# Kernel optimization log

Hardware: AMD Instinct MI355X
Metric: run time of the kernel (lower is better)

The kernel has to match this reference:

```python
import jax, jax.numpy as jnp
import numpy as np

NUM_HEADS = 16

def setup_inputs() -> dict:
    key = jax.random.key(0)
    ks = jax.random.split(key, 5)
    b, c, w, h = 2, 1024, 48, 48
    sc = 0.02
    return {
        "x": jax.random.normal(ks[0], (b, c, w, h), jnp.float32),
        "Wqkv": jax.random.normal(ks[1], (3 * c, c), jnp.float32) * sc,
        "bqkv": jax.random.normal(ks[2], (3 * c,), jnp.float32) * sc,
        "Wo": jax.random.normal(ks[3], (c, c), jnp.float32) * sc,
        "bo": jax.random.normal(ks[4], (c,), jnp.float32) * sc,
    }

def reference(x, Wqkv, bqkv, Wo, bo):
    b, c, w, h = x.shape
    n = NUM_HEADS
    hd = c // n
    s = w * h
    # [b,c,w,h] -> tokens [b, s, c]
    xs = x.transpose(0, 2, 3, 1).reshape(b, s, c)
    qkv = xs @ Wqkv.T + bqkv                       # [b, s, 3c]
    # rearrange 'b s (three n hd) -> three b n s hd'
    qkv = qkv.reshape(b, s, 3, n, hd).transpose(2, 0, 3, 1, 4)
    q, k, v = qkv[0], qkv[1], qkv[2]               # [b, n, s, hd]
    score = jnp.einsum('bnqh,bnkh->bnqk', q, k) / jnp.sqrt(jnp.float32(hd))
    # module uses a soft causal mask: subtract 10000 above the diagonal
    mask = 10000.0 * jnp.triu(jnp.ones((s, s), dtype=score.dtype), k=1)
    attn = jax.nn.softmax(score - mask, axis=-1)   # [b, n, s, s]
    z = jnp.einsum('bnqk,bnkh->bqnh', attn, v).reshape(b, s, c)
    out = z @ Wo.T + bo                            # [b, s, c]
    return out.reshape(b, w, h, c).transpose(0, 3, 1, 2)
```

## Files before the change

kernel.cpp:

```cpp
#include <hip/hip_runtime.h>

typedef __bf16 bf16;
typedef __bf16 bf16x8 __attribute__((ext_vector_type(8)));
typedef float floatx4 __attribute__((ext_vector_type(4)));
typedef float floatx16 __attribute__((ext_vector_type(16)));

static constexpr int S = 2304;
static constexpr int C = 1024;
static constexpr int NHEAD = 16;
static constexpr int HDIM = 64;
static constexpr int BATCH = 2;
static constexpr float QSCALE = 0.18033688011112042f;
static constexpr int QSPLIT = 18;
static constexpr int NACC = S - QSPLIT * 64;

__global__ __launch_bounds__(256) void k_zero(float4* __restrict__ p, int n4) {
  int i = blockIdx.x * 256 + threadIdx.x;
  if (i < n4) p[i] = float4{0.f, 0.f, 0.f, 0.f};
}

__global__ __launch_bounds__(256) void k_convert(const float* __restrict__ src,
                                                 bf16* __restrict__ dst, int n8) {
  int i = blockIdx.x * 256 + threadIdx.x;
  if (i >= n8) return;
  float4 a = *(const float4*)(src + (size_t)i * 8);
  float4 b = *(const float4*)(src + (size_t)i * 8 + 4);
  bf16x8 o;
  o[0] = (bf16)a.x; o[1] = (bf16)a.y; o[2] = (bf16)a.z; o[3] = (bf16)a.w;
  o[4] = (bf16)b.x; o[5] = (bf16)b.y; o[6] = (bf16)b.z; o[7] = (bf16)b.w;
  *(bf16x8*)(dst + (size_t)i * 8) = o;
}

__global__ __launch_bounds__(256) void k_transpose(const float* __restrict__ x,
                                                   bf16* __restrict__ xs) {
  __shared__ bf16 T[64 * 72];
  int c0 = blockIdx.x * 64, t0 = blockIdx.y * 64, b = blockIdx.z;
  int tid = threadIdx.x;
  const float* xb = x + (size_t)b * C * S;
#pragma unroll
  for (int it = 0; it < 4; ++it) {
    int idx = it * 256 + tid;
    int rc = idx >> 4, t4 = idx & 15;
    float4 v = *(const float4*)(xb + (size_t)(c0 + rc) * S + t0 + t4 * 4);
    T[(t4 * 4 + 0) * 72 + rc] = (bf16)v.x;
    T[(t4 * 4 + 1) * 72 + rc] = (bf16)v.y;
    T[(t4 * 4 + 2) * 72 + rc] = (bf16)v.z;
    T[(t4 * 4 + 3) * 72 + rc] = (bf16)v.w;
  }
  __syncthreads();
  bf16* xsb = xs + (size_t)b * S * C;
#pragma unroll
  for (int it = 0; it < 2; ++it) {
    int idx = it * 256 + tid;
    int rt = idx >> 3, c8 = idx & 7;
    bf16x8 v;
#pragma unroll
    for (int i = 0; i < 8; ++i) v[i] = T[rt * 72 + c8 * 8 + i];
    *(bf16x8*)(xsb + (size_t)(t0 + rt) * C + c0 + c8 * 8) = v;
  }
}

__device__ __forceinline__ void g2l16(const bf16* g, bf16* l) {
  __builtin_amdgcn_global_load_lds(
      (const __attribute__((address_space(1))) void*)g,
      (__attribute__((address_space(3))) void*)l, 16, 0, 0);
}

__device__ __forceinline__ unsigned cvtpk(float a, float b) {
  unsigned r;
  asm("v_cvt_pk_bf16_f32 %0, %1, %2" : "=v"(r) : "v"(a), "v"(b));
  return r;
}

__device__ __forceinline__ void pl32(unsigned& a, unsigned& b) {
  asm("v_permlane32_swap_b32 %0, %1" : "+v"(a), "+v"(b));
}

template <int EPI>
__global__ __launch_bounds__(256) void k_gemm_bt(const bf16* __restrict__ A,
                                                 const bf16* __restrict__ Bt,
                                                 const float* __restrict__ bias,
                                                 bf16* __restrict__ q,
                                                 bf16* __restrict__ k,
                                                 bf16* __restrict__ v,
                                                 float* __restrict__ outf) {
  constexpr int K = C;
  __shared__ bf16 As[128 * 64];
  __shared__ bf16 Bs[128 * 64];
  int tid = threadIdx.x;
  int w = tid >> 6, lane = tid & 63, ln = lane & 15, quad = lane >> 4;
  int m0 = blockIdx.y * 128, n0 = blockIdx.x * 128;
  int moff = (w >> 1) * 64, noff = (w & 1) * 64;
  floatx4 acc[4][4] = {};

  int sr[4], sc[4];
#pragma unroll
  for (int it = 0; it < 4; ++it) {
    int L = (it * 4 + w) * 64 + lane;
    sr[it] = L >> 3;
    sc[it] = (L & 7) ^ (sr[it] & 7);
  }

  for (int k0 = 0; k0 < K; k0 += 64) {
    __syncthreads();
#pragma unroll
    for (int it = 0; it < 4; ++it) {
      int cb = (it * 4 + w) * 64;
      g2l16(A + (size_t)(m0 + sr[it]) * K + k0 + sc[it] * 8, As + cb * 8);
      g2l16(Bt + (size_t)(n0 + sr[it]) * K + k0 + sc[it] * 8, Bs + cb * 8);
    }
    __syncthreads();
#pragma unroll
    for (int t = 0; t < 2; ++t) {
      bf16x8 af[4], bfr[4];
#pragma unroll
      for (int i = 0; i < 4; ++i) {
        int ra = moff + i * 16 + ln;
        af[i]  = *(const bf16x8*)(As + ra * 64 + (((t * 4 + quad) ^ (ra & 7))) * 8);
        int rb = noff + i * 16 + ln;
        bfr[i] = *(const bf16x8*)(Bs + rb * 64 + (((t * 4 + quad) ^ (rb & 7))) * 8);
      }
#pragma unroll
      for (int im = 0; im < 4; ++im)
#pragma unroll
        for (int in = 0; in < 4; ++in)
          acc[im][in] = __builtin_amdgcn_mfma_f32_16x16x32_bf16(
              af[im], bfr[in], acc[im][in], 0, 0, 0);
    }
  }

  int bidx = (m0 >= S) ? 1 : 0;
  if (EPI == 0) {
#pragma unroll
    for (int in = 0; in < 4; ++in) {
      int j = n0 + noff + in * 16 + ln;
      float bv = bias[j];
      int three = j >> 10;
      int head = (j >> 6) & 15;
      int hdi = j & 63;
#pragma unroll
      for (int im = 0; im < 4; ++im) {
        int mbase = m0 + moff + im * 16 + quad * 4;
        int tb = mbase - bidx * S;
        if (three == 2) {
          union { ushort4 u; bf16 h[4]; } P;
#pragma unroll
          for (int r = 0; r < 4; ++r) P.h[r] = (bf16)(acc[im][in][r] + bv);
          *(ushort4*)(v + ((size_t)(bidx * NHEAD + head) * HDIM + hdi) * S + tb) = P.u;
        } else if (three == 0) {
          bf16* dst = q + ((size_t)(bidx * NHEAD + head) * S + tb) * HDIM + hdi;
#pragma unroll
          for (int r = 0; r < 4; ++r)
            dst[(size_t)r * HDIM] = (bf16)((acc[im][in][r] + bv) * QSCALE);
        } else {
          bf16* dst = k + ((size_t)(bidx * NHEAD + head) * S + tb) * HDIM + hdi;
#pragma unroll
          for (int r = 0; r < 4; ++r) dst[(size_t)r * HDIM] = (bf16)(acc[im][in][r] + bv);
        }
      }
    }
  } else {
#pragma unroll
    for (int in = 0; in < 4; ++in) {
      int co = n0 + noff + in * 16 + ln;
      float bv = bias[co];
#pragma unroll
      for (int im = 0; im < 4; ++im) {
        int mbase = m0 + moff + im * 16 + quad * 4;
        int tb = mbase - bidx * S;
        float4 st;
        st.x = acc[im][in][0] + bv;
        st.y = acc[im][in][1] + bv;
        st.z = acc[im][in][2] + bv;
        st.w = acc[im][in][3] + bv;
        *(float4*)(outf + ((size_t)bidx * C + co) * S + tb) = st;
      }
    }
  }
}

__global__ __launch_bounds__(256) void k_attn_part(const bf16* __restrict__ Qg,
                                                   const bf16* __restrict__ Kg,
                                                   const bf16* __restrict__ Vtg,
                                                   bf16* __restrict__ z,
                                                   float* __restrict__ Oacc,
                                                   float* __restrict__ Lacc) {
  __shared__ bf16 Ks[2][64 * 64];
  __shared__ bf16 Vs[2][64 * 64];
  int i = blockIdx.x;
  int xcd = i & 7, j = i >> 3;
  int grp = j / 27, r = j % 27;
  int bh = xcd + 8 * grp;
  int qi, lo, hi;
  bool single = (r >= 18);
  if (!single) {
    qi = 17 - (r >> 1);
    lo = (r & 1) * (qi + 1);
    hi = lo + qi + 1;
  } else {
    qi = 26 - r;
    lo = 0;
    hi = 2 * qi + 2;
  }
  int b = bh >> 4, h = bh & 15;
  int tid = threadIdx.x;
  int w = tid >> 6, lane = tid & 63;
  int ql = lane & 31, hw = lane >> 5;
  int q0 = qi * 128;
  int qw = q0 + w * 32;
  int qg = qw + ql;
  int ktd = qw >> 6;

  const bf16* kb = Kg + (size_t)bh * S * HDIM;
  const bf16* vb = Vtg + (size_t)bh * HDIM * S;

  int s_row = tid >> 3;
  int s_c8 = (tid & 7) ^ (s_row & 7);
  size_t kOff1 = (size_t)s_row * HDIM + s_c8 * 8;
  size_t kOff2 = kOff1 + (size_t)32 * HDIM;
  size_t vOff1 = (size_t)s_row * S + s_c8 * 8;
  size_t vOff2 = vOff1 + (size_t)32 * S;

  const bf16* qb = Qg + ((size_t)bh * S + qg) * HDIM + hw * 8;
  bf16x8 qf[4];
#pragma unroll
  for (int c = 0; c < 4; ++c) qf[c] = *(const bf16x8*)(qb + c * 16);

  float lsum = 0.f;
  floatx16 o0 = {}, o1 = {};

  const bf16* kb0 = kb + (size_t)lo * 64 * HDIM;
  const bf16* vb0 = vb + (size_t)lo * 64;
  g2l16(kb0 + kOff1, Ks[0] + tid * 8);
  g2l16(kb0 + kOff2, Ks[0] + (256 + tid) * 8);
  g2l16(vb0 + vOff1, Vs[0] + tid * 8);
  g2l16(vb0 + vOff2, Vs[0] + (256 + tid) * 8);

  const bf16* kbn = kb0 + (size_t)64 * HDIM;
  const bf16* vbn = vb0 + 64;

  int qsw = ql & 7;

#pragma unroll 1
  for (int kt = lo; kt < hi; ++kt) {
    int cur = (kt - lo) & 1;
    __syncthreads();

    if (kt + 1 < hi) {
      bf16* kd = Ks[1 - cur];
      bf16* vd = Vs[1 - cur];
      g2l16(kbn + kOff1, kd + tid * 8);
      g2l16(kbn + kOff2, kd + (256 + tid) * 8);
      g2l16(vbn + vOff1, vd + tid * 8);
      g2l16(vbn + vOff2, vd + (256 + tid) * 8);
      kbn += (size_t)64 * HDIM;
      vbn += 64;
    }

    if (kt > ktd) continue;
    bool diag = (kt == ktd);

    const bf16* ksb = Ks[cur];
    const bf16* vsb = Vs[cur];

    floatx16 sa0 = {}, sa1 = {};
    __builtin_amdgcn_s_setprio(1);
#pragma unroll
    for (int c = 0; c < 4; ++c) {
      int c8 = ((2 * c + hw) ^ qsw) * 8;
      bf16x8 k0 = *(const bf16x8*)(ksb + ql * 64 + c8);
      bf16x8 k1 = *(const bf16x8*)(ksb + (32 + ql) * 64 + c8);
      sa0 = __builtin_amdgcn_mfma_f32_32x32x16_bf16(k0, qf[c], sa0, 0, 0, 0);
      sa1 = __builtin_amdgcn_mfma_f32_32x32x16_bf16(k1, qf[c], sa1, 0, 0, 0);
    }
    __builtin_amdgcn_s_setprio(0);

    unsigned pk0[8], pk1[8];
    if (!diag) {
#pragma unroll
      for (int t = 0; t < 8; ++t) {
        float a = exp2f(sa0[2 * t]), c2 = exp2f(sa0[2 * t + 1]);
        float d = exp2f(sa1[2 * t]), e = exp2f(sa1[2 * t + 1]);
        lsum += (a + c2) + (d + e);
        pk0[t] = cvtpk(a, c2);
        pk1[t] = cvtpk(d, e);
      }
    } else {
      int qd = qg - kt * 64;
#pragma unroll
      for (int t = 0; t < 8; ++t) {
        int r0 = 2 * t, r1 = 2 * t + 1;
        int k0l = (r0 & 3) + 8 * (r0 >> 2) + 4 * hw;
        int k1l = (r1 & 3) + 8 * (r1 >> 2) + 4 * hw;
        float a = (k0l > qd) ? 0.f : exp2f(sa0[r0]);
        float c2 = (k1l > qd) ? 0.f : exp2f(sa0[r1]);
        float d = (32 + k0l > qd) ? 0.f : exp2f(sa1[r0]);
        float e = (32 + k1l > qd) ? 0.f : exp2f(sa1[r1]);
        lsum += (a + c2) + (d + e);
        pk0[t] = cvtpk(a, c2);
        pk1[t] = cvtpk(d, e);
      }
    }

    __builtin_amdgcn_s_setprio(1);
#pragma unroll
    for (int ktc = 0; ktc < 4; ++ktc) {
      unsigned d0, d1, d2, d3;
      if (ktc == 0)      { d0 = pk0[0]; d1 = pk0[1]; d2 = pk0[2]; d3 = pk0[3]; }
      else if (ktc == 1) { d0 = pk0[4]; d1 = pk0[5]; d2 = pk0[6]; d3 = pk0[7]; }
      else if (ktc == 2) { d0 = pk1[0]; d1 = pk1[1]; d2 = pk1[2]; d3 = pk1[3]; }
      else               { d0 = pk1[4]; d1 = pk1[5]; d2 = pk1[6]; d3 = pk1[7]; }
      pl32(d0, d2);
      pl32(d1, d3);
      union { unsigned u[4]; bf16x8 v; } pf;
      pf.u[0] = d0; pf.u[1] = d1; pf.u[2] = d2; pf.u[3] = d3;
      int c8 = ((2 * ktc + hw) ^ qsw) * 8;
      bf16x8 v0 = *(const bf16x8*)(vsb + ql * 64 + c8);
      bf16x8 v1 = *(const bf16x8*)(vsb + (32 + ql) * 64 + c8);
      o0 = __builtin_amdgcn_mfma_f32_32x32x16_bf16(v0, pf.v, o0, 0, 0, 0);
      o1 = __builtin_amdgcn_mfma_f32_32x32x16_bf16(v1, pf.v, o1, 0, 0, 0);
    }
    __builtin_amdgcn_s_setprio(0);
  }

  lsum += __shfl_xor(lsum, 32);

  if (single) {
    float inv = 1.f / lsum;
    bf16* dst = z + ((size_t)b * S + qg) * C + h * HDIM + 4 * hw;
#pragma unroll
    for (int hdblk = 0; hdblk < 2; ++hdblk) {
#pragma unroll
      for (int rg = 0; rg < 4; ++rg) {
        union { ushort4 u; bf16 hh[4]; } P;
#pragma unroll
        for (int jj = 0; jj < 4; ++jj) {
          float ov = hdblk ? o1[rg * 4 + jj] : o0[rg * 4 + jj];
          P.hh[jj] = (bf16)(ov * inv);
        }
        *(ushort4*)(dst + hdblk * 32 + rg * 8) = P.u;
      }
    }
  } else {
    int qa = qg - QSPLIT * 64;
    if (hw == 0) atomicAdd(&Lacc[bh * NACC + qa], lsum);
#pragma unroll
    for (int hdblk = 0; hdblk < 2; ++hdblk) {
#pragma unroll
      for (int rr = 0; rr < 16; ++rr) {
        int hd = hdblk * 32 + (rr & 3) + 8 * (rr >> 2) + 4 * hw;
        float ov = hdblk ? o1[rr] : o0[rr];
        atomicAdd(&Oacc[((size_t)bh * 64 + hd) * NACC + qa], ov);
      }
    }
  }
}

__global__ __launch_bounds__(256) void k_norm(const float* __restrict__ Oacc,
                                              const float* __restrict__ Lacc,
                                              bf16* __restrict__ z) {
  __shared__ float T[64 * 65];
  int qt = blockIdx.x, bh = blockIdx.y;
  int b = bh >> 4, h = bh & 15;
  int qrel0 = qt * 64;
  int q0 = QSPLIT * 64 + qrel0;
  int tid = threadIdx.x;
  int q4 = (tid & 15) * 4, hd0 = tid >> 4;
  float4 lv = *(const float4*)(Lacc + bh * NACC + qrel0 + q4);
  float inv0 = 1.f / lv.x, inv1 = 1.f / lv.y, inv2 = 1.f / lv.z, inv3 = 1.f / lv.w;
#pragma unroll
  for (int hf = 0; hf < 4; ++hf) {
    int hd = hf * 16 + hd0;
    float4 v = *(const float4*)(Oacc + ((size_t)bh * 64 + hd) * NACC + qrel0 + q4);
    T[(q4 + 0) * 65 + hd] = v.x * inv0;
    T[(q4 + 1) * 65 + hd] = v.y * inv1;
    T[(q4 + 2) * 65 + hd] = v.z * inv2;
    T[(q4 + 3) * 65 + hd] = v.w * inv3;
  }
  __syncthreads();
#pragma unroll
  for (int it = 0; it < 2; ++it) {
    int idx = it * 256 + tid;
    int qq = idx >> 3, c8 = idx & 7;
    bf16x8 o;
#pragma unroll
    for (int k = 0; k < 8; ++k) o[k] = (bf16)T[qq * 65 + c8 * 8 + k];
    *(bf16x8*)(z + ((size_t)b * S + q0 + qq) * C + h * HDIM + c8 * 8) = o;
  }
}

extern "C" void kernel_launch(void* const* d_in, const int* in_sizes, int n_in,
                              void* d_out, int out_size, void* d_ws, size_t ws_size,
                              hipStream_t stream) {
  const float* x    = (const float*)d_in[0];
  const float* Wqkv = (const float*)d_in[1];
  const float* bqkv = (const float*)d_in[2];
  const float* Wo   = (const float*)d_in[3];
  const float* bo   = (const float*)d_in[4];
  float* out = (float*)d_out;

  bf16* ws = (bf16*)d_ws;
  const size_t tok = (size_t)BATCH * S * C;
  bf16* xs   = ws;
  bf16* Qg   = ws + tok;
  bf16* Kg   = ws + 2 * tok;
  bf16* Vtg  = ws + 3 * tok;
  bf16* Wqb  = ws + 4 * tok;
  bf16* Wob  = Wqb + (size_t)3 * C * C;
  float* Oacc = (float*)(Wob + (size_t)C * C);
  float* Lacc = Oacc + (size_t)32 * 64 * NACC;
  bf16* z    = xs;

  k_zero<<<2340, 256, 0, stream>>>((float4*)Oacc, 599040);
  k_convert<<<(3 * C * C / 8 + 255) / 256, 256, 0, stream>>>(Wqkv, Wqb, 3 * C * C / 8);
  k_convert<<<(C * C / 8 + 255) / 256, 256, 0, stream>>>(Wo, Wob, C * C / 8);
  k_transpose<<<dim3(C / 64, S / 64, BATCH), 256, 0, stream>>>(x, xs);
  k_gemm_bt<0><<<dim3(3 * C / 128, BATCH * S / 128), 256, 0, stream>>>(
      xs, Wqb, bqkv, Qg, Kg, Vtg, nullptr);
  k_attn_part<<<dim3(864), 256, 0, stream>>>(Qg, Kg, Vtg, z, Oacc, Lacc);
  k_norm<<<dim3(18, 32), 256, 0, stream>>>(Oacc, Lacc, z);
  k_gemm_bt<1><<<dim3(C / 128, BATCH * S / 128), 256, 0, stream>>>(
      z, Wob, bo, nullptr, nullptr, nullptr, out);
}
```

Measured before the change: 224.8 us.

## Use 512-thread attention blocks with table-driven causal split of KV ranges

The attention kernel moves from 256-thread blocks covering 128 query rows to 512-thread blocks covering 256 query rows. Each thread now issues a single async load per K and V tile instead of two. The per-block query tile and KV range come from lookup tables that split long causal rows into several partial chunks, balancing work across 31 jobs per head. The row-sum accumulator is split into two independent chains to shorten dependencies. QSPLIT changes so more rows use the partial-accumulate path, which enlarges the zeroing and the normalization kernel.

```diff
diff --git a/kernel.cpp b/kernel.cpp
--- a/kernel.cpp
+++ b/kernel.cpp
@@ -11,7 +11,7 @@
 static constexpr int HDIM = 64;
 static constexpr int BATCH = 2;
 static constexpr float QSCALE = 0.18033688011112042f;
-static constexpr int QSPLIT = 18;
+static constexpr int QSPLIT = 12;
 static constexpr int NACC = S - QSPLIT * 64;
 
 __global__ __launch_bounds__(256) void k_zero(float4* __restrict__ p, int n4) {
@@ -179,7 +179,7 @@
   }
 }
 
-__global__ __launch_bounds__(256) void k_attn_part(const bf16* __restrict__ Qg,
+__global__ __launch_bounds__(512) void k_attn_part(const bf16* __restrict__ Qg,
                                                    const bf16* __restrict__ Kg,
                                                    const bf16* __restrict__ Vtg,
                                                    bf16* __restrict__ z,
@@ -187,27 +187,23 @@
                                                    float* __restrict__ Lacc) {
   __shared__ bf16 Ks[2][64 * 64];
   __shared__ bf16 Vs[2][64 * 64];
+  static const unsigned char QT[31] = {2,1,8,8,8,8,8,8,7,7,6,6,6,5,5,5,5,3,
+                                       7,7,7,7,6,6,4,4,4,4,3,3,0};
+  static const unsigned char LO[31] = {0,0,0,6,12,18,24,30,0,6,0,6,12,0,6,12,18,0,
+                                       12,17,22,27,18,23,0,5,10,15,6,11,0};
+  static const unsigned char HI[31] = {12,8,6,12,18,24,30,36,6,12,6,12,18,6,12,18,24,6,
+                                       17,22,27,32,23,28,5,10,15,20,11,16,4};
   int i = blockIdx.x;
   int xcd = i & 7, j = i >> 3;
-  int grp = j / 27, r = j % 27;
+  int grp = j / 31, r = j % 31;
   int bh = xcd + 8 * grp;
-  int qi, lo, hi;
-  bool single = (r >= 18);
-  if (!single) {
-    qi = 17 - (r >> 1);
-    lo = (r & 1) * (qi + 1);
-    hi = lo + qi + 1;
-  } else {
-    qi = 26 - r;
-    lo = 0;
-    hi = 2 * qi + 2;
-  }
+  int qt = QT[r], lo = LO[r], hi = HI[r];
+  bool single = (qt <= 2);
   int b = bh >> 4, h = bh & 15;
   int tid = threadIdx.x;
   int w = tid >> 6, lane = tid & 63;
   int ql = lane & 31, hw = lane >> 5;
-  int q0 = qi * 128;
-  int qw = q0 + w * 32;
+  int qw = qt * 256 + w * 32;
   int qg = qw + ql;
   int ktd = qw >> 6;
 
@@ -216,25 +212,21 @@
 
   int s_row = tid >> 3;
   int s_c8 = (tid & 7) ^ (s_row & 7);
-  size_t kOff1 = (size_t)s_row * HDIM + s_c8 * 8;
-  size_t kOff2 = kOff1 + (size_t)32 * HDIM;
-  size_t vOff1 = (size_t)s_row * S + s_c8 * 8;
-  size_t vOff2 = vOff1 + (size_t)32 * S;
+  size_t kOff = (size_t)s_row * HDIM + s_c8 * 8;
+  size_t vOff = (size_t)s_row * S + s_c8 * 8;
 
   const bf16* qb = Qg + ((size_t)bh * S + qg) * HDIM + hw * 8;
   bf16x8 qf[4];
 #pragma unroll
   for (int c = 0; c < 4; ++c) qf[c] = *(const bf16x8*)(qb + c * 16);
 
-  float lsum = 0.f;
+  float lsA = 0.f, lsB = 0.f;
   floatx16 o0 = {}, o1 = {};
 
   const bf16* kb0 = kb + (size_t)lo * 64 * HDIM;
   const bf16* vb0 = vb + (size_t)lo * 64;
-  g2l16(kb0 + kOff1, Ks[0] + tid * 8);
-  g2l16(kb0 + kOff2, Ks[0] + (256 + tid) * 8);
-  g2l16(vb0 + vOff1, Vs[0] + tid * 8);
-  g2l16(vb0 + vOff2, Vs[0] + (256 + tid) * 8);
+  g2l16(kb0 + kOff, Ks[0] + tid * 8);
+  g2l16(vb0 + vOff, Vs[0] + tid * 8);
 
   const bf16* kbn = kb0 + (size_t)64 * HDIM;
   const bf16* vbn = vb0 + 64;
@@ -247,12 +239,8 @@
     __syncthreads();
 
     if (kt + 1 < hi) {
-      bf16* kd = Ks[1 - cur];
-      bf16* vd = Vs[1 - cur];
-      g2l16(kbn + kOff1, kd + tid * 8);
-      g2l16(kbn + kOff2, kd + (256 + tid) * 8);
-      g2l16(vbn + vOff1, vd + tid * 8);
-      g2l16(vbn + vOff2, vd + (256 + tid) * 8);
+      g2l16(kbn + kOff, Ks[1 - cur] + tid * 8);
+      g2l16(vbn + vOff, Vs[1 - cur] + tid * 8);
       kbn += (size_t)64 * HDIM;
       vbn += 64;
     }
@@ -281,7 +269,8 @@
       for (int t = 0; t < 8; ++t) {
         float a = exp2f(sa0[2 * t]), c2 = exp2f(sa0[2 * t + 1]);
         float d = exp2f(sa1[2 * t]), e = exp2f(sa1[2 * t + 1]);
-        lsum += (a + c2) + (d + e);
+        lsA += a + c2;
+        lsB += d + e;
         pk0[t] = cvtpk(a, c2);
         pk1[t] = cvtpk(d, e);
       }
@@ -296,7 +285,8 @@
         float c2 = (k1l > qd) ? 0.f : exp2f(sa0[r1]);
         float d = (32 + k0l > qd) ? 0.f : exp2f(sa1[r0]);
         float e = (32 + k1l > qd) ? 0.f : exp2f(sa1[r1]);
-        lsum += (a + c2) + (d + e);
+        lsA += a + c2;
+        lsB += d + e;
         pk0[t] = cvtpk(a, c2);
         pk1[t] = cvtpk(d, e);
       }
@@ -323,6 +313,7 @@
     __builtin_amdgcn_s_setprio(0);
   }
 
+  float lsum = lsA + lsB;
   lsum += __shfl_xor(lsum, 32);
 
   if (single) {
@@ -411,14 +402,14 @@
   float* Lacc = Oacc + (size_t)32 * 64 * NACC;
   bf16* z    = xs;
 
-  k_zero<<<2340, 256, 0, stream>>>((float4*)Oacc, 599040);
+  k_zero<<<3120, 256, 0, stream>>>((float4*)Oacc, 798720);
   k_convert<<<(3 * C * C / 8 + 255) / 256, 256, 0, stream>>>(Wqkv, Wqb, 3 * C * C / 8);
   k_convert<<<(C * C / 8 + 255) / 256, 256, 0, stream>>>(Wo, Wob, C * C / 8);
   k_transpose<<<dim3(C / 64, S / 64, BATCH), 256, 0, stream>>>(x, xs);
   k_gemm_bt<0><<<dim3(3 * C / 128, BATCH * S / 128), 256, 0, stream>>>(
       xs, Wqb, bqkv, Qg, Kg, Vtg, nullptr);
-  k_attn_part<<<dim3(864), 256, 0, stream>>>(Qg, Kg, Vtg, z, Oacc, Lacc);
-  k_norm<<<dim3(18, 32), 256, 0, stream>>>(Oacc, Lacc, z);
+  k_attn_part<<<dim3(992), 512, 0, stream>>>(Qg, Kg, Vtg, z, Oacc, Lacc);
+  k_norm<<<dim3(24, 32), 256, 0, stream>>>(Oacc, Lacc, z);
   k_gemm_bt<1><<<dim3(C / 128, BATCH * S / 128), 256, 0, stream>>>(
       z, Wob, bo, nullptr, nullptr, nullptr, out);
 }
```

Measured after the change: 229.2 us. Within noise of the previous version (+2.0%).
